# Kernel optimization log

Measured on AMD Instinct MI355X. Metric: run time of the kernel, lower is better.

## Reference

```python
import jax, jax.numpy as jnp
import numpy as np

N, D_IN, D_OUT = 1024, 512, 128
DROP_P = 0.4


def setup_inputs() -> dict:
    key = jax.random.key(0)
    k1, k2, k3, k4, kw, kb = jax.random.split(key, 6)
    inp = {
        "x1": jax.random.normal(k1, (N, D_IN), dtype=jnp.float32),
        "x2": jax.random.normal(k2, (N, D_IN), dtype=jnp.float32),
        "x3": jax.random.normal(k3, (N, D_IN), dtype=jnp.float32),
        "x4": jax.random.normal(k4, (N, D_IN), dtype=jnp.float32),
        # Linear(D_IN, D_OUT): torch stores weight as [out, in]
        "W": jax.random.normal(kw, (D_OUT, D_IN), dtype=jnp.float32) * (1.0 / np.sqrt(D_IN)),
        "b": jax.random.normal(kb, (D_OUT,), dtype=jnp.float32) * 0.01,
    }
    return inp


def reference(x1, x2, x3, x4, W, b):
    lin = lambda x: x @ W.T + b            # shared Linear, [N, D_OUT]
    q = lin(x1)
    k = lin(x2)
    v = lin(x3)
    scale = lin(x4)                         # [N, D]
    # softmax over dim=0 (across rows), then unsqueeze(-1) -> [N, D, 1]
    inv_scale = jax.nn.softmax(scale, axis=0)[..., None]
    qk = q @ k.T                            # [N, N]
    # broadcast divide: [N,1,N] / [N,D,1] -> [N, D, N]
    scaled_qk = qk[:, None, :] / inv_scale
    softmax_qk = jax.nn.softmax(scaled_qk, axis=-1)
    # dropout p=0.4 (training mode), deterministic key for reproducibility
    keep = jax.random.bernoulli(jax.random.key(42), 1.0 - DROP_P, softmax_qk.shape)
    dropout_qk = jnp.where(keep, softmax_qk / (1.0 - DROP_P), 0.0)
    # torch broadcast matmul: [N,D,N] @ [N,D] -> [N,D,D]
    output = jnp.einsum('ndm,mk->ndk', dropout_qk, v)
    return output
```

## Files before the change

### kernel.cpp

```cpp
#include <hip/hip_runtime.h>
#include <stdint.h>
#include <math.h>

static constexpr int NN  = 1024;
static constexpr int DIN = 512;
static constexpr int DD  = 128;

__device__ __forceinline__ uint32_t rotl32(uint32_t x, uint32_t r) {
  return (x << r) | (x >> (32u - r));
}

__device__ __forceinline__ bool keep_mask(uint32_t idx) {
  uint32_t x0 = 0u, x1 = idx;
  const uint32_t k0 = 0u, k1 = 42u;
  const uint32_t k2 = k0 ^ k1 ^ 0x1BD11BDAu;
  x0 += k0; x1 += k1;
#define TF_ROUND(r) { x0 += x1; x1 = rotl32(x1, r); x1 ^= x0; }
  TF_ROUND(13u) TF_ROUND(15u) TF_ROUND(26u) TF_ROUND(6u)
  x0 += k1; x1 += k2 + 1u;
  TF_ROUND(17u) TF_ROUND(29u) TF_ROUND(16u) TF_ROUND(24u)
  x0 += k2; x1 += k0 + 2u;
  TF_ROUND(13u) TF_ROUND(15u) TF_ROUND(26u) TF_ROUND(6u)
  x0 += k0; x1 += k1 + 3u;
  TF_ROUND(17u) TF_ROUND(29u) TF_ROUND(16u) TF_ROUND(24u)
  x0 += k1; x1 += k2 + 4u;
  TF_ROUND(13u) TF_ROUND(15u) TF_ROUND(26u) TF_ROUND(6u)
  x0 += k2; x1 += k0 + 5u;
#undef TF_ROUND
  const uint32_t bits = x0 ^ x1;
  const float u = __uint_as_float((bits >> 9) | 0x3f800000u) - 1.0f;
  return u < 0.6f;
}

__global__ __launch_bounds__(256) void wtrans_kernel(
    const float* __restrict__ W, float* __restrict__ WTp) {
  const int t = threadIdx.x;
  const int d = blockIdx.x * 2 + (t >> 7);
  const int k4 = t & 127;
  const float4 w = *(const float4*)&W[d * DIN + k4 * 4];
  *(float4*)&WTp[(size_t)k4 * (DD * 4) + d * 4] = w;
}

__global__ __launch_bounds__(256) void lin_kernel(
    const float* __restrict__ x1, const float* __restrict__ x2,
    const float* __restrict__ x3, const float* __restrict__ x4,
    const float* __restrict__ WTp, const float* __restrict__ bias,
    float* __restrict__ q, float* __restrict__ kk,
    float* __restrict__ v, float* __restrict__ sc) {
  __shared__ float Xs[8 * 516];
  const int t = threadIdx.x;
  const int n0 = blockIdx.x * 8;
  const int mat = blockIdx.y;
  const float* x = (mat == 0) ? x1 : (mat == 1) ? x2 : (mat == 2) ? x3 : x4;
  float* o = (mat == 0) ? q : (mat == 1) ? kk : (mat == 2) ? v : sc;

#pragma unroll
  for (int it = 0; it < 4; ++it) {
    const int i = t + 256 * it;
    const int r = i >> 7, c = (i & 127) * 4;
    *(float4*)&Xs[r * 516 + c] = *(const float4*)&x[(size_t)(n0 + r) * DIN + c];
  }
  __syncthreads();

  const int d = t & 127;
  const int g2 = t >> 7;
  float acc[4] = {0.f, 0.f, 0.f, 0.f};
  const float* wp = &WTp[d * 4];

#pragma unroll 4
  for (int k4 = 0; k4 < 128; ++k4) {
    const float4 w4 = *(const float4*)&wp[(size_t)k4 * (DD * 4)];
#pragma unroll
    for (int j = 0; j < 4; ++j) {
      const float4 xa = *(const float4*)&Xs[(g2 * 4 + j) * 516 + k4 * 4];
      acc[j] = fmaf(xa.x, w4.x, fmaf(xa.y, w4.y,
               fmaf(xa.z, w4.z, fmaf(xa.w, w4.w, acc[j]))));
    }
  }

  const float bd = bias[d];
#pragma unroll
  for (int j = 0; j < 4; ++j)
    o[(size_t)(n0 + g2 * 4 + j) * DD + d] = acc[j] + bd;
}

__global__ __launch_bounds__(256) void mid_kernel(
    const float* __restrict__ q, const float* __restrict__ kref,
    const float* __restrict__ sc, float* __restrict__ qkout,
    float* __restrict__ inv) {
  const int t = threadIdx.x;
  if (blockIdx.x < 256) {
    __shared__ float qs[64 * 132];
    __shared__ float ks[64 * 132];
    const int tx = t & 15, ty = t >> 4;
    const int tm = (blockIdx.x & 15) * 64, tn = (blockIdx.x >> 4) * 64;
    for (int it = 0; it < 8; ++it) {
      const int i = t + 256 * it;
      const int r = i >> 5, c = (i & 31) * 4;
      *(float4*)&qs[r * 132 + c] = *(const float4*)&q[(tn + r) * DD + c];
      *(float4*)&ks[r * 132 + c] = *(const float4*)&kref[(tm + r) * DD + c];
    }
    __syncthreads();
    float acc[4][4] = {};
    for (int k0 = 0; k0 < DD; k0 += 4) {
      float4 qv[4], kv[4];
#pragma unroll
      for (int i = 0; i < 4; ++i) qv[i] = *(const float4*)&qs[(ty * 4 + i) * 132 + k0];
#pragma unroll
      for (int j = 0; j < 4; ++j) kv[j] = *(const float4*)&ks[(tx + 16 * j) * 132 + k0];
#pragma unroll
      for (int i = 0; i < 4; ++i)
#pragma unroll
        for (int j = 0; j < 4; ++j)
          acc[i][j] = fmaf(qv[i].x, kv[j].x,
                      fmaf(qv[i].y, kv[j].y,
                      fmaf(qv[i].z, kv[j].z,
                      fmaf(qv[i].w, kv[j].w, acc[i][j]))));
    }
#pragma unroll
    for (int i = 0; i < 4; ++i)
#pragma unroll
      for (int j = 0; j < 4; ++j)
        qkout[(size_t)(tn + ty * 4 + i) * NN + tm + tx + 16 * j] = acc[i][j];
  } else {
    __shared__ float red[256];
    const int d = blockIdx.x - 256;
    float vals[4];
    float mx = -INFINITY;
#pragma unroll
    for (int i = 0; i < 4; ++i) {
      vals[i] = sc[(size_t)(t + 256 * i) * DD + d];
      mx = fmaxf(mx, vals[i]);
    }
    red[t] = mx; __syncthreads();
    for (int s = 128; s > 0; s >>= 1) {
      if (t < s) red[t] = fmaxf(red[t], red[t + s]);
      __syncthreads();
    }
    mx = red[0]; __syncthreads();
    float e[4]; float sm = 0.f;
#pragma unroll
    for (int i = 0; i < 4; ++i) { e[i] = expf(vals[i] - mx); sm += e[i]; }
    red[t] = sm; __syncthreads();
    for (int s = 128; s > 0; s >>= 1) {
      if (t < s) red[t] += red[t + s];
      __syncthreads();
    }
    sm = red[0];
#pragma unroll
    for (int i = 0; i < 4; ++i)
      inv[(size_t)(t + 256 * i) * DD + d] = e[i] / sm;
  }
}

__global__ __launch_bounds__(256) void attn_kernel(
    const float* __restrict__ qk, const float* __restrict__ inv_scale,
    const float* __restrict__ v, float* __restrict__ out) {
  __shared__ float qkrow[NN];
  __shared__ float red[8];
  __shared__ int   surv[NN];
  __shared__ float Pl[16][130];
  __shared__ float Vs[16][132];
  __shared__ float sdv[DD];
  __shared__ float rsl[DD];
  __shared__ int   cnt;

  const int n = blockIdx.x;
  const int t = threadIdx.x;

  const float4 q4 = *(const float4*)&qk[(size_t)n * NN + t * 4];
  *(float4*)&qkrow[t * 4] = q4;
  float mx = fmaxf(fmaxf(q4.x, q4.y), fmaxf(q4.z, q4.w));
#pragma unroll
  for (int o = 32; o > 0; o >>= 1) mx = fmaxf(mx, __shfl_xor(mx, o));
  if ((t & 63) == 0) red[t >> 6] = mx;
  float iv = 0.f;
  if (t < DD) { iv = inv_scale[n * DD + t]; sdv[t] = 1.0f / iv; }
  float miv = iv;
#pragma unroll
  for (int o = 32; o > 0; o >>= 1) miv = fmaxf(miv, __shfl_xor(miv, o));
  if ((t & 63) == 0) red[4 + (t >> 6)] = miv;
  if (t == 0) cnt = 0;
  __syncthreads();
  const float qkmax = fmaxf(fmaxf(red[0], red[1]), fmaxf(red[2], red[3]));
  const float maxinv = fmaxf(red[4], red[5]);
  const float th = qkmax - 30.f * maxinv;

  {
    const float qv[4] = {q4.x, q4.y, q4.z, q4.w};
#pragma unroll
    for (int j = 0; j < 4; ++j)
      if (qv[j] > th) { const int p = atomicAdd(&cnt, 1); surv[p] = t * 4 + j; }
  }
  __syncthreads();
  const int K = cnt;

  const int k4 = (t & 31) * 4;
  const int dbase = t >> 5;
  float4 acc4[16];
#pragma unroll
  for (int g = 0; g < 16; ++g) acc4[g] = make_float4(0.f, 0.f, 0.f, 0.f);
  float Sloc = 0.f;

  for (int c0 = 0; c0 < K; c0 += 16) {
    const int C = min(16, K - c0);
    __syncthreads();
    if (t < DD) {
      const float sd = sdv[t];
      const uint32_t dg = ((uint32_t)(n * DD + t)) << 10;
      for (int s = 0; s < C; ++s) {
        const int m = surv[c0 + s];
        const float arg = (qkrow[m] - qkmax) * sd;
        const float e = __expf(arg);
        Sloc += e;
        float p = 0.f;
        if (arg > -30.f) {
          if (keep_mask(dg + (uint32_t)m)) p = e;
        }
        Pl[s][t] = p;
      }
    } else {
      const int u = t - 128;
      for (int slot = u; slot < C * 32; slot += 128) {
        const int s = slot >> 5, c = (slot & 31) * 4;
        *(float4*)&Vs[s][c] = *(const float4*)&v[(size_t)surv[c0 + s] * DD + c];
      }
    }
    __syncthreads();
    for (int s = 0; s < C; ++s) {
      const float4 vv = *(const float4*)&Vs[s][k4];
#pragma unroll
      for (int g = 0; g < 16; ++g) {
        const float p = Pl[s][g * 8 + dbase];
        acc4[g].x = fmaf(p, vv.x, acc4[g].x);
        acc4[g].y = fmaf(p, vv.y, acc4[g].y);
        acc4[g].z = fmaf(p, vv.z, acc4[g].z);
        acc4[g].w = fmaf(p, vv.w, acc4[g].w);
      }
    }
  }

  __syncthreads();
  if (t < DD) rsl[t] = 1.0f / (Sloc * 0.6f);
  __syncthreads();
  float* op = &out[(size_t)n * (DD * DD) + t * 4];
#pragma unroll
  for (int g = 0; g < 16; ++g) {
    const float rs = rsl[g * 8 + dbase];
    float4 r = acc4[g];
    r.x *= rs; r.y *= rs; r.z *= rs; r.w *= rs;
    *(float4*)&op[g * 1024] = r;
  }
}

extern "C" void kernel_launch(void* const* d_in, const int* in_sizes, int n_in,
                              void* d_out, int out_size, void* d_ws, size_t ws_size,
                              hipStream_t stream) {
  const float* x1 = (const float*)d_in[0];
  const float* x2 = (const float*)d_in[1];
  const float* x3 = (const float*)d_in[2];
  const float* x4 = (const float*)d_in[3];
  const float* W  = (const float*)d_in[4];
  const float* b  = (const float*)d_in[5];
  float* out = (float*)d_out;

  float* ws   = (float*)d_ws;
  float* q    = ws;
  float* k    = ws + 131072;
  float* v    = ws + 262144;
  float* sc   = ws + 393216;
  float* inv  = ws + 524288;
  float* qkm  = ws + 655360;
  float* WTp  = ws + 1703936;

  wtrans_kernel<<<dim3(64), 256, 0, stream>>>(W, WTp);
  lin_kernel<<<dim3(128, 4), 256, 0, stream>>>(x1, x2, x3, x4, WTp, b, q, k, v, sc);
  mid_kernel<<<dim3(384), 256, 0, stream>>>(q, k, sc, qkm, inv);
  attn_kernel<<<NN, 256, 0, stream>>>(qkm, inv, v, out);
}
```

Baseline: 117.4 us.

## Fuse all four kernels into one persistent kernel with grid barriers

Replaces the four separate launches (W transpose, linear, qk/softmax, attention) with one persistent kernel of 512 blocks that separates the phases with software grid barriers built on atomics. This removes launch gaps and per-kernel ramp-up. The qk tile is now loaded in two k-halves to fit a shared memory buffer, and each block handles two attention rows. The risks are deadlock if not all 512 blocks are co-resident, barrier spin cost, and half the block count in the attention phase.

```diff
diff --git a/kernel.cpp b/kernel.cpp
--- a/kernel.cpp
+++ b/kernel.cpp
@@ -5,6 +5,29 @@
 static constexpr int NN  = 1024;
 static constexpr int DIN = 512;
 static constexpr int DD  = 128;
+static constexpr int NBLK = 512;
+
+__device__ unsigned g_cnt[4];
+__device__ unsigned g_gen[4];
+
+__device__ __forceinline__ void grid_barrier(int i) {
+  __syncthreads();
+  if (threadIdx.x == 0) {
+    __threadfence();
+    unsigned g = __hip_atomic_load(&g_gen[i], __ATOMIC_RELAXED, __HIP_MEMORY_SCOPE_AGENT);
+    unsigned a = __hip_atomic_fetch_add(&g_cnt[i], 1u, __ATOMIC_ACQ_REL, __HIP_MEMORY_SCOPE_AGENT);
+    if (a == (unsigned)(NBLK - 1)) {
+      __hip_atomic_store(&g_cnt[i], 0u, __ATOMIC_RELAXED, __HIP_MEMORY_SCOPE_AGENT);
+      __hip_atomic_fetch_add(&g_gen[i], 1u, __ATOMIC_RELEASE, __HIP_MEMORY_SCOPE_AGENT);
+    } else {
+      while (__hip_atomic_load(&g_gen[i], __ATOMIC_RELAXED, __HIP_MEMORY_SCOPE_AGENT) == g) {
+        __builtin_amdgcn_s_sleep(2);
+      }
+    }
+    __threadfence();
+  }
+  __syncthreads();
+}
 
 __device__ __forceinline__ uint32_t rotl32(uint32_t x, uint32_t r) {
   return (x << r) | (x >> (32u - r));
@@ -32,99 +55,103 @@
   return u < 0.6f;
 }
 
-__global__ __launch_bounds__(256) void wtrans_kernel(
-    const float* __restrict__ W, float* __restrict__ WTp) {
-  const int t = threadIdx.x;
-  const int d = blockIdx.x * 2 + (t >> 7);
-  const int k4 = t & 127;
-  const float4 w = *(const float4*)&W[d * DIN + k4 * 4];
-  *(float4*)&WTp[(size_t)k4 * (DD * 4) + d * 4] = w;
-}
-
-__global__ __launch_bounds__(256) void lin_kernel(
+__global__ __launch_bounds__(256, 2) void fused_all(
     const float* __restrict__ x1, const float* __restrict__ x2,
     const float* __restrict__ x3, const float* __restrict__ x4,
-    const float* __restrict__ WTp, const float* __restrict__ bias,
-    float* __restrict__ q, float* __restrict__ kk,
-    float* __restrict__ v, float* __restrict__ sc) {
-  __shared__ float Xs[8 * 516];
+    const float* __restrict__ W,  const float* __restrict__ bias,
+    float* __restrict__ q, float* __restrict__ kk, float* __restrict__ v,
+    float* __restrict__ sc, float* __restrict__ inv, float* __restrict__ qkm,
+    float* __restrict__ WTp, float* __restrict__ out) {
+  __shared__ __align__(16) float smem[8704];
   const int t = threadIdx.x;
-  const int n0 = blockIdx.x * 8;
-  const int mat = blockIdx.y;
-  const float* x = (mat == 0) ? x1 : (mat == 1) ? x2 : (mat == 2) ? x3 : x4;
-  float* o = (mat == 0) ? q : (mat == 1) ? kk : (mat == 2) ? v : sc;
-
-#pragma unroll
-  for (int it = 0; it < 4; ++it) {
-    const int i = t + 256 * it;
-    const int r = i >> 7, c = (i & 127) * 4;
-    *(float4*)&Xs[r * 516 + c] = *(const float4*)&x[(size_t)(n0 + r) * DIN + c];
-  }
-  __syncthreads();
-
-  const int d = t & 127;
-  const int g2 = t >> 7;
-  float acc[4] = {0.f, 0.f, 0.f, 0.f};
-  const float* wp = &WTp[d * 4];
-
+  const int bid = blockIdx.x;
+
+  {
+    const int gid = bid * 256 + t;
+    if (gid < 16384) {
+      const int d = gid >> 7, k4 = gid & 127;
+      *(float4*)&WTp[(size_t)k4 * (DD * 4) + d * 4] =
+          *(const float4*)&W[(size_t)d * DIN + k4 * 4];
+    }
+  }
+  grid_barrier(0);
+
+  {
+    float* Xs = smem;
+    const int n0 = (bid & 127) * 8;
+    const int mat = bid >> 7;
+    const float* x = (mat == 0) ? x1 : (mat == 1) ? x2 : (mat == 2) ? x3 : x4;
+    float* o = (mat == 0) ? q : (mat == 1) ? kk : (mat == 2) ? v : sc;
+#pragma unroll
+    for (int it = 0; it < 4; ++it) {
+      const int i = t + 256 * it;
+      const int r = i >> 7, c = (i & 127) * 4;
+      *(float4*)&Xs[r * 516 + c] = *(const float4*)&x[(size_t)(n0 + r) * DIN + c];
+    }
+    __syncthreads();
+    const int d = t & 127;
+    const int g2 = t >> 7;
+    float acc[4] = {0.f, 0.f, 0.f, 0.f};
+    const float* wp = &WTp[d * 4];
 #pragma unroll 4
-  for (int k4 = 0; k4 < 128; ++k4) {
-    const float4 w4 = *(const float4*)&wp[(size_t)k4 * (DD * 4)];
-#pragma unroll
-    for (int j = 0; j < 4; ++j) {
-      const float4 xa = *(const float4*)&Xs[(g2 * 4 + j) * 516 + k4 * 4];
-      acc[j] = fmaf(xa.x, w4.x, fmaf(xa.y, w4.y,
-               fmaf(xa.z, w4.z, fmaf(xa.w, w4.w, acc[j]))));
-    }
-  }
-
-  const float bd = bias[d];
-#pragma unroll
-  for (int j = 0; j < 4; ++j)
-    o[(size_t)(n0 + g2 * 4 + j) * DD + d] = acc[j] + bd;
-}
-
-__global__ __launch_bounds__(256) void mid_kernel(
-    const float* __restrict__ q, const float* __restrict__ kref,
-    const float* __restrict__ sc, float* __restrict__ qkout,
-    float* __restrict__ inv) {
-  const int t = threadIdx.x;
-  if (blockIdx.x < 256) {
-    __shared__ float qs[64 * 132];
-    __shared__ float ks[64 * 132];
+    for (int k4 = 0; k4 < 128; ++k4) {
+      const float4 w4 = *(const float4*)&wp[(size_t)k4 * (DD * 4)];
+#pragma unroll
+      for (int j = 0; j < 4; ++j) {
+        const float4 xa = *(const float4*)&Xs[(g2 * 4 + j) * 516 + k4 * 4];
+        acc[j] = fmaf(xa.x, w4.x, fmaf(xa.y, w4.y,
+                 fmaf(xa.z, w4.z, fmaf(xa.w, w4.w, acc[j]))));
+      }
+    }
+    const float bd = bias[d];
+#pragma unroll
+    for (int j = 0; j < 4; ++j)
+      o[(size_t)(n0 + g2 * 4 + j) * DD + d] = acc[j] + bd;
+  }
+  grid_barrier(1);
+
+  if (bid < 256) {
+    float* qs = smem;
+    float* ks = smem + 4352;
     const int tx = t & 15, ty = t >> 4;
-    const int tm = (blockIdx.x & 15) * 64, tn = (blockIdx.x >> 4) * 64;
-    for (int it = 0; it < 8; ++it) {
-      const int i = t + 256 * it;
-      const int r = i >> 5, c = (i & 31) * 4;
-      *(float4*)&qs[r * 132 + c] = *(const float4*)&q[(tn + r) * DD + c];
-      *(float4*)&ks[r * 132 + c] = *(const float4*)&kref[(tm + r) * DD + c];
-    }
-    __syncthreads();
+    const int tm = (bid & 15) * 64, tn = (bid >> 4) * 64;
     float acc[4][4] = {};
-    for (int k0 = 0; k0 < DD; k0 += 4) {
-      float4 qv[4], kv[4];
-#pragma unroll
-      for (int i = 0; i < 4; ++i) qv[i] = *(const float4*)&qs[(ty * 4 + i) * 132 + k0];
-#pragma unroll
-      for (int j = 0; j < 4; ++j) kv[j] = *(const float4*)&ks[(tx + 16 * j) * 132 + k0];
-#pragma unroll
-      for (int i = 0; i < 4; ++i)
-#pragma unroll
-        for (int j = 0; j < 4; ++j)
-          acc[i][j] = fmaf(qv[i].x, kv[j].x,
-                      fmaf(qv[i].y, kv[j].y,
-                      fmaf(qv[i].z, kv[j].z,
-                      fmaf(qv[i].w, kv[j].w, acc[i][j]))));
-    }
-#pragma unroll
-    for (int i = 0; i < 4; ++i)
+    for (int kp = 0; kp < 2; ++kp) {
+      __syncthreads();
+#pragma unroll
+      for (int it = 0; it < 4; ++it) {
+        const int i = t + 256 * it;
+        const int rr = i >> 4, cc = (i & 15) * 4;
+        *(float4*)&qs[rr * 68 + cc] =
+            *(const float4*)&q[(size_t)(tn + rr) * DD + kp * 64 + cc];
+        *(float4*)&ks[rr * 68 + cc] =
+            *(const float4*)&kk[(size_t)(tm + rr) * DD + kp * 64 + cc];
+      }
+      __syncthreads();
+      for (int k0 = 0; k0 < 64; k0 += 4) {
+        float4 qv[4], kv[4];
+#pragma unroll
+        for (int i2 = 0; i2 < 4; ++i2) qv[i2] = *(const float4*)&qs[(ty * 4 + i2) * 68 + k0];
+#pragma unroll
+        for (int j = 0; j < 4; ++j) kv[j] = *(const float4*)&ks[(tx + 16 * j) * 68 + k0];
+#pragma unroll
+        for (int i2 = 0; i2 < 4; ++i2)
+#pragma unroll
+          for (int j = 0; j < 4; ++j)
+            acc[i2][j] = fmaf(qv[i2].x, kv[j].x,
+                         fmaf(qv[i2].y, kv[j].y,
+                         fmaf(qv[i2].z, kv[j].z,
+                         fmaf(qv[i2].w, kv[j].w, acc[i2][j]))));
+      }
+    }
+#pragma unroll
+    for (int i2 = 0; i2 < 4; ++i2)
 #pragma unroll
       for (int j = 0; j < 4; ++j)
-        qkout[(size_t)(tn + ty * 4 + i) * NN + tm + tx + 16 * j] = acc[i][j];
-  } else {
-    __shared__ float red[256];
-    const int d = blockIdx.x - 256;
+        qkm[(size_t)(tn + ty * 4 + i2) * NN + tm + tx + 16 * j] = acc[i2][j];
+  } else if (bid < 384) {
+    float* red2 = smem;
+    const int d = bid - 256;
     float vals[4];
     float mx = -INFINITY;
 #pragma unroll
@@ -132,124 +159,124 @@
       vals[i] = sc[(size_t)(t + 256 * i) * DD + d];
       mx = fmaxf(mx, vals[i]);
     }
-    red[t] = mx; __syncthreads();
+    red2[t] = mx; __syncthreads();
     for (int s = 128; s > 0; s >>= 1) {
-      if (t < s) red[t] = fmaxf(red[t], red[t + s]);
-      __syncthreads();
-    }
-    mx = red[0]; __syncthreads();
+      if (t < s) red2[t] = fmaxf(red2[t], red2[t + s]);
+      __syncthreads();
+    }
+    mx = red2[0]; __syncthreads();
     float e[4]; float sm = 0.f;
 #pragma unroll
     for (int i = 0; i < 4; ++i) { e[i] = expf(vals[i] - mx); sm += e[i]; }
-    red[t] = sm; __syncthreads();
+    red2[t] = sm; __syncthreads();
     for (int s = 128; s > 0; s >>= 1) {
-      if (t < s) red[t] += red[t + s];
-      __syncthreads();
-    }
-    sm = red[0];
+      if (t < s) red2[t] += red2[t + s];
+      __syncthreads();
+    }
+    sm = red2[0];
 #pragma unroll
     for (int i = 0; i < 4; ++i)
       inv[(size_t)(t + 256 * i) * DD + d] = e[i] / sm;
   }
-}
-
-__global__ __launch_bounds__(256) void attn_kernel(
-    const float* __restrict__ qk, const float* __restrict__ inv_scale,
-    const float* __restrict__ v, float* __restrict__ out) {
-  __shared__ float qkrow[NN];
-  __shared__ float red[8];
-  __shared__ int   surv[NN];
-  __shared__ float Pl[16][130];
-  __shared__ float Vs[16][132];
-  __shared__ float sdv[DD];
-  __shared__ float rsl[DD];
-  __shared__ int   cnt;
-
-  const int n = blockIdx.x;
-  const int t = threadIdx.x;
-
-  const float4 q4 = *(const float4*)&qk[(size_t)n * NN + t * 4];
-  *(float4*)&qkrow[t * 4] = q4;
-  float mx = fmaxf(fmaxf(q4.x, q4.y), fmaxf(q4.z, q4.w));
-#pragma unroll
-  for (int o = 32; o > 0; o >>= 1) mx = fmaxf(mx, __shfl_xor(mx, o));
-  if ((t & 63) == 0) red[t >> 6] = mx;
-  float iv = 0.f;
-  if (t < DD) { iv = inv_scale[n * DD + t]; sdv[t] = 1.0f / iv; }
-  float miv = iv;
-#pragma unroll
-  for (int o = 32; o > 0; o >>= 1) miv = fmaxf(miv, __shfl_xor(miv, o));
-  if ((t & 63) == 0) red[4 + (t >> 6)] = miv;
-  if (t == 0) cnt = 0;
-  __syncthreads();
-  const float qkmax = fmaxf(fmaxf(red[0], red[1]), fmaxf(red[2], red[3]));
-  const float maxinv = fmaxf(red[4], red[5]);
-  const float th = qkmax - 30.f * maxinv;
+  grid_barrier(2);
 
   {
-    const float qv[4] = {q4.x, q4.y, q4.z, q4.w};
-#pragma unroll
-    for (int j = 0; j < 4; ++j)
-      if (qv[j] > th) { const int p = atomicAdd(&cnt, 1); surv[p] = t * 4 + j; }
-  }
-  __syncthreads();
-  const int K = cnt;
-
-  const int k4 = (t & 31) * 4;
-  const int dbase = t >> 5;
-  float4 acc4[16];
-#pragma unroll
-  for (int g = 0; g < 16; ++g) acc4[g] = make_float4(0.f, 0.f, 0.f, 0.f);
-  float Sloc = 0.f;
-
-  for (int c0 = 0; c0 < K; c0 += 16) {
-    const int C = min(16, K - c0);
-    __syncthreads();
-    if (t < DD) {
-      const float sd = sdv[t];
-      const uint32_t dg = ((uint32_t)(n * DD + t)) << 10;
-      for (int s = 0; s < C; ++s) {
-        const int m = surv[c0 + s];
-        const float arg = (qkrow[m] - qkmax) * sd;
-        const float e = __expf(arg);
-        Sloc += e;
-        float p = 0.f;
-        if (arg > -30.f) {
-          if (keep_mask(dg + (uint32_t)m)) p = e;
+    float* qkrow = smem;
+    int*   surv  = (int*)(smem + 1024);
+    float* Pl    = smem + 2048;
+    float* Vs    = smem + 4128;
+    float* sdv   = smem + 6240;
+    float* rsl   = smem + 6368;
+    float* red   = smem + 6496;
+    int*   cnt   = (int*)(smem + 6504);
+
+    for (int rrow = 0; rrow < 2; ++rrow) {
+      const int n = bid * 2 + rrow;
+      __syncthreads();
+      const float4 q4 = *(const float4*)&qkm[(size_t)n * NN + t * 4];
+      *(float4*)&qkrow[t * 4] = q4;
+      float mx = fmaxf(fmaxf(q4.x, q4.y), fmaxf(q4.z, q4.w));
+#pragma unroll
+      for (int o2 = 32; o2 > 0; o2 >>= 1) mx = fmaxf(mx, __shfl_xor(mx, o2));
+      if ((t & 63) == 0) red[t >> 6] = mx;
+      float iv = 0.f;
+      if (t < DD) { iv = inv[n * DD + t]; sdv[t] = 1.0f / iv; }
+      float miv = iv;
+#pragma unroll
+      for (int o2 = 32; o2 > 0; o2 >>= 1) miv = fmaxf(miv, __shfl_xor(miv, o2));
+      if ((t & 63) == 0) red[4 + (t >> 6)] = miv;
+      if (t == 0) *cnt = 0;
+      __syncthreads();
+      const float qkmax = fmaxf(fmaxf(red[0], red[1]), fmaxf(red[2], red[3]));
+      const float maxinv = fmaxf(red[4], red[5]);
+      const float th = qkmax - 30.f * maxinv;
+      {
+        const float qv2[4] = {q4.x, q4.y, q4.z, q4.w};
+#pragma unroll
+        for (int j = 0; j < 4; ++j)
+          if (qv2[j] > th) { const int p = atomicAdd(cnt, 1); surv[p] = t * 4 + j; }
+      }
+      __syncthreads();
+      const int K = *cnt;
+
+      const int k4 = (t & 31) * 4;
+      const int dbase = t >> 5;
+      float4 acc4[16];
+#pragma unroll
+      for (int g = 0; g < 16; ++g) acc4[g] = make_float4(0.f, 0.f, 0.f, 0.f);
+      float Sloc = 0.f;
+
+      for (int c0 = 0; c0 < K; c0 += 16) {
+        const int C = min(16, K - c0);
+        __syncthreads();
+        if (t < DD) {
+          const float sd = sdv[t];
+          const uint32_t dg = ((uint32_t)(n * DD + t)) << 10;
+          for (int s = 0; s < C; ++s) {
+            const int m = surv[c0 + s];
+            const float arg = (qkrow[m] - qkmax) * sd;
+            const float e = __expf(arg);
+            Sloc += e;
+            float p = 0.f;
+            if (arg > -30.f) {
+              if (keep_mask(dg + (uint32_t)m)) p = e;
+            }
+            Pl[s * 130 + t] = p;
+          }
+        } else {
+          const int u = t - 128;
+          for (int slot = u; slot < C * 32; slot += 128) {
+            const int s = slot >> 5, c = (slot & 31) * 4;
+            *(float4*)&Vs[s * 132 + c] =
+                *(const float4*)&v[(size_t)surv[c0 + s] * DD + c];
+          }
         }
-        Pl[s][t] = p;
-      }
-    } else {
-      const int u = t - 128;
-      for (int slot = u; slot < C * 32; slot += 128) {
-        const int s = slot >> 5, c = (slot & 31) * 4;
-        *(float4*)&Vs[s][c] = *(const float4*)&v[(size_t)surv[c0 + s] * DD + c];
-      }
-    }
-    __syncthreads();
-    for (int s = 0; s < C; ++s) {
-      const float4 vv = *(const float4*)&Vs[s][k4];
+        __syncthreads();
+        for (int s = 0; s < C; ++s) {
+          const float4 vv = *(const float4*)&Vs[s * 132 + k4];
+#pragma unroll
+          for (int g = 0; g < 16; ++g) {
+            const float p = Pl[s * 130 + g * 8 + dbase];
+            acc4[g].x = fmaf(p, vv.x, acc4[g].x);
+            acc4[g].y = fmaf(p, vv.y, acc4[g].y);
+            acc4[g].z = fmaf(p, vv.z, acc4[g].z);
+            acc4[g].w = fmaf(p, vv.w, acc4[g].w);
+          }
+        }
+      }
+
+      __syncthreads();
+      if (t < DD) rsl[t] = 1.0f / (Sloc * 0.6f);
+      __syncthreads();
+      float* op = &out[(size_t)n * (DD * DD) + t * 4];
 #pragma unroll
       for (int g = 0; g < 16; ++g) {
-        const float p = Pl[s][g * 8 + dbase];
-        acc4[g].x = fmaf(p, vv.x, acc4[g].x);
-        acc4[g].y = fmaf(p, vv.y, acc4[g].y);
-        acc4[g].z = fmaf(p, vv.z, acc4[g].z);
-        acc4[g].w = fmaf(p, vv.w, acc4[g].w);
-      }
-    }
-  }
-
-  __syncthreads();
-  if (t < DD) rsl[t] = 1.0f / (Sloc * 0.6f);
-  __syncthreads();
-  float* op = &out[(size_t)n * (DD * DD) + t * 4];
-#pragma unroll
-  for (int g = 0; g < 16; ++g) {
-    const float rs = rsl[g * 8 + dbase];
-    float4 r = acc4[g];
-    r.x *= rs; r.y *= rs; r.z *= rs; r.w *= rs;
-    *(float4*)&op[g * 1024] = r;
+        const float rs = rsl[g * 8 + dbase];
+        float4 r2 = acc4[g];
+        r2.x *= rs; r2.y *= rs; r2.z *= rs; r2.w *= rs;
+        *(float4*)&op[g * 1024] = r2;
+      }
+    }
   }
 }
 
@@ -273,8 +300,6 @@
   float* qkm  = ws + 655360;
   float* WTp  = ws + 1703936;
 
-  wtrans_kernel<<<dim3(64), 256, 0, stream>>>(W, WTp);
-  lin_kernel<<<dim3(128, 4), 256, 0, stream>>>(x1, x2, x3, x4, WTp, b, q, k, v, sc);
-  mid_kernel<<<dim3(384), 256, 0, stream>>>(q, k, sc, qkm, inv);
-  attn_kernel<<<NN, 256, 0, stream>>>(qkm, inv, v, out);
-}
+  fused_all<<<dim3(NBLK), dim3(256), 0, stream>>>(
+      x1, x2, x3, x4, W, b, q, k, v, sc, inv, qkm, WTp, out);
+}
```

Measured after the change: 209.1 us. +78.1%, slower.
